# Kernel tuning notes

Hardware: AMD Instinct MI355X
Metric: run time of the kernel (lower is better)

## Reference

```python
import jax, jax.numpy as jnp
import numpy as np

F_BINS, NCH, NSRC, W, H, T, B = 257, 8, 2, 5, 32, 2000, 4
PAD = (W - 1) // 2  # use_pad=True


def setup_inputs() -> dict:
    key = jax.random.key(0)
    ks = jax.random.split(key, 7)
    s = 0.05
    return {
        "x": jax.random.normal(ks[0], (B, 2 * F_BINS, NCH, T), dtype=jnp.float32),
        # per-frequency depthwise complex conv weights: (F, Cout, Cin, w)
        "Wr1": jax.random.normal(ks[1], (F_BINS, H, NCH, W), dtype=jnp.float32) * s,
        "Wi1": jax.random.normal(ks[2], (F_BINS, H, NCH, W), dtype=jnp.float32) * s,
        "Wr2": jax.random.normal(ks[3], (F_BINS, H, H, W), dtype=jnp.float32) * s,
        "Wi2": jax.random.normal(ks[4], (F_BINS, H, H, W), dtype=jnp.float32) * s,
        "Wr3": jax.random.normal(ks[5], (F_BINS, NCH * NSRC, H, W), dtype=jnp.float32) * s,
        "Wi3": jax.random.normal(ks[6], (F_BINS, NCH * NSRC, H, W), dtype=jnp.float32) * s,
    }


def _dwconv(z, Wt):
    # z: (B, F, Cin, T) treated as NCHW with C=F, H=Cin, W=T
    # Wt: (F, Cout, Cin, w) -> grouped conv with groups=F, kernel spans full Cin
    f, cout, cin, w = Wt.shape
    k = Wt.reshape(f * cout, 1, cin, w)
    y = jax.lax.conv_general_dilated(
        z, k, window_strides=(1, 1), padding=[(0, 0), (PAD, PAD)],
        feature_group_count=f, dimension_numbers=("NCHW", "OIHW", "NCHW"))
    b = z.shape[0]
    return y.reshape(b, f, cout, -1)  # (B, F, Cout, T)


def _cconv(zr, zi, Wr, Wi):
    # complex conv: (Wr + i Wi) * (zr + i zi)
    hr = _dwconv(zr, Wr) - _dwconv(zi, Wi)
    hi = _dwconv(zr, Wi) + _dwconv(zi, Wr)
    return hr, hi


def reference(x, Wr1, Wi1, Wr2, Wi2, Wr3, Wi3):
    xr, xi = jnp.split(x, 2, axis=1)  # each (B, F, nCH, T)
    h1r, h1i = _cconv(xr, xi, Wr1, Wi1)
    h1r, h1i = jax.nn.relu(h1r), jax.nn.relu(h1i)
    h2r, h2i = _cconv(h1r, h1i, Wr2, Wi2)
    h2r, h2i = jax.nn.relu(h2r), jax.nn.relu(h2i)
    h3r, h3i = _cconv(h2r, h2i, Wr3, Wi3)  # (B, F, nCH*nSource, T)
    b, f, _, t = xr.shape
    hr = h3r.reshape(b, f, NCH, NSRC, t)
    hi = h3i.reshape(b, f, NCH, NSRC, t)
    # broadcast-multiply and reduce over channels (nCH)
    yrr = jnp.einsum("bfct,bfcst->bfst", xr, hr)
    yri = jnp.einsum("bfct,bfcst->bfst", xr, hi)
    yir = jnp.einsum("bfct,bfcst->bfst", xi, hr)
    yii = jnp.einsum("bfct,bfcst->bfst", xi, hi)
    Yr = yrr - yii
    Yi = yri + yir
    out = jnp.concatenate((Yr, Yi), axis=1)  # (B, 2F, nSource, T); squeeze is a no-op for B>1
    return jnp.squeeze(out)
```

## Files before the change

### kernel.cpp

```cpp
#include <hip/hip_runtime.h>

#define F_BINS 257
#define NCH    8
#define NSRC   2
#define KW     5
#define HCH    32
#define TLEN   2000
#define BATCH  4

#define TT      128
#define NTILES  16

#define XSTRIDE 24
#define XCOLS   148
#define XOFF    0
#define XSZ     (XCOLS * XSTRIDE * 2)
#define HWIN    144
#define H1OFF   XSZ
#define HSZ     (HWIN * 64 * 2)
#define H2OFF   (H1OFF + HSZ)
#define SMEM_BYTES (H2OFF + HSZ)
#define H3OFF   H1OFF
#define H3STRIDE 40

#define NFRAG   36
#define PW_HALF8_PER_F (NFRAG * 2 * 64)
#define PW_BYTES ((size_t)F_BINS * PW_HALF8_PER_F * 16)

typedef _Float16 half8  __attribute__((ext_vector_type(8)));
typedef __fp16   pk16x2 __attribute__((ext_vector_type(2)));
typedef float    f32x4  __attribute__((ext_vector_type(4)));

#define MFMA16(a, b, c) __builtin_amdgcn_mfma_f32_16x16x32_f16(a, b, c, 0, 0, 0)

__device__ __forceinline__ half8 gather_frag(
    int f, int frag, int mw, int lane,
    const float* __restrict__ Wr1, const float* __restrict__ Wi1,
    const float* __restrict__ Wr2, const float* __restrict__ Wi2,
    const float* __restrict__ Wr3, const float* __restrict__ Wi3)
{
    const int g = lane >> 4, r16 = lane & 15;
    half8 v;
    if (frag < 6) {
        int hr = frag / 3, p = frag % 3;
        int tap = 2 * p + (g >> 1);
        #pragma unroll
        for (int j = 0; j < 8; ++j) {
            float val = 0.f;
            if (tap < KW) {
                long idx = (((long)f * HCH + hr * 16 + r16) * NCH + j) * KW + tap;
                if (mw == 0) val = (g & 1) ? -Wi1[idx] : Wr1[idx];
                else         val = (g & 1) ?  Wr1[idx] : Wi1[idx];
            }
            v[j] = (_Float16)val;
        }
    } else if (frag < 26) {
        int u = frag - 6;
        int w = u >> 2, hr = (u >> 1) & 1, kk = u & 1;
        #pragma unroll
        for (int j = 0; j < 8; ++j) {
            int c = g * 8 + j;
            long idx = (((long)f * HCH + hr * 16 + r16) * HCH + c) * KW + w;
            float val;
            if (mw == 0) val = kk ? -Wi2[idx] : Wr2[idx];
            else         val = kk ?  Wr2[idx] : Wi2[idx];
            v[j] = (_Float16)val;
        }
    } else {
        int u = frag - 26;
        int w = u >> 1, kk = u & 1;
        #pragma unroll
        for (int j = 0; j < 8; ++j) {
            int c = g * 8 + j;
            long idx = (((long)f * (NCH * NSRC) + r16) * HCH + c) * KW + w;
            float val;
            if (mw == 0) val = kk ? -Wi3[idx] : Wr3[idx];
            else         val = kk ?  Wr3[idx] : Wi3[idx];
            v[j] = (_Float16)val;
        }
    }
    return v;
}

__global__ __launch_bounds__(256) void repack_kernel(
    const float* __restrict__ Wr1, const float* __restrict__ Wi1,
    const float* __restrict__ Wr2, const float* __restrict__ Wi2,
    const float* __restrict__ Wr3, const float* __restrict__ Wi3,
    _Float16* __restrict__ pw)
{
    const int bid  = blockIdx.x;
    const int f    = bid >> 2;
    const int part = bid & 3;
    const int lane = threadIdx.x & 63;
    const int q    = threadIdx.x >> 6;
    half8* pwv = (half8*)pw;
    for (int u = part * 18 + q; u < part * 18 + 18; u += 4) {
        int frag = u >> 1, mw = u & 1;
        half8 v = gather_frag(f, frag, mw, lane, Wr1, Wi1, Wr2, Wi2, Wr3, Wi3);
        pwv[((size_t)f * (NFRAG * 2) + u) * 64 + lane] = v;
    }
}

template<bool PACKED>
__global__ __launch_bounds__(256, 3) void cddcnn_mfma_kernel(
    const float* __restrict__ x,
    const float* __restrict__ Wr1, const float* __restrict__ Wi1,
    const float* __restrict__ Wr2, const float* __restrict__ Wi2,
    const float* __restrict__ Wr3, const float* __restrict__ Wi3,
    float* __restrict__ out, const _Float16* __restrict__ pw)
{
    __shared__ __align__(16) char sm[SMEM_BYTES];

    const int tid  = threadIdx.x;
    const int lane = tid & 63;
    const int wv   = tid >> 6;
    const int mw   = wv >> 1;
    const int nw   = wv & 1;
    const int g    = lane >> 4;
    const int r16  = lane & 15;

    const int bid = blockIdx.x;
    const int tl  = bid % NTILES;
    const int f   = (bid / NTILES) % F_BINS;
    const int b   = bid / (NTILES * F_BINS);
    const int t0  = tl * TT;

    const int nb0 = nw ? 5 : 0;
    const int nbn = nw ? 4 : 5;

    const half8* pwf = PACKED ? ((const half8*)pw) + (size_t)f * PW_HALF8_PER_F + mw * 64 + lane
                              : nullptr;
    #define LOADFRAG(fr) (PACKED ? pwf[(fr) * 128] \
                                 : gather_frag(f, (fr), mw, lane, Wr1, Wi1, Wr2, Wi2, Wr3, Wi3))

    const long xr_base = ((long)(b * 2 * F_BINS + f) * NCH) * TLEN;
    const long xi_base = ((long)(b * 2 * F_BINS + F_BINS + f) * NCH) * TLEN;

    half8 a1[2][3];
    #pragma unroll
    for (int hr = 0; hr < 2; ++hr)
    #pragma unroll
    for (int p = 0; p < 3; ++p)
        a1[hr][p] = LOADFRAG(hr * 3 + p);

    for (int u = tid; u < 16 * 37; u += 256) {
        int pc  = u / 37;
        int q   = u - pc * 37;
        int idx = q * 4;
        int tt  = t0 - 10 + idx;
        long base = (pc < 8) ? (xr_base + (long)pc * TLEN)
                             : (xi_base + (long)(pc - 8) * TLEN);
        char* wp = sm + XOFF + (idx * XSTRIDE + pc) * 2;
        #pragma unroll
        for (int h = 0; h < 2; ++h) {
            int t2 = tt + 2 * h;
            float v0 = 0.f, v1 = 0.f;
            if (t2 >= 0 && t2 + 1 < TLEN) {
                float2 xx = *(const float2*)(x + base + t2);
                v0 = xx.x; v1 = xx.y;
            } else {
                if (t2 >= 0 && t2 < TLEN)         v0 = x[base + t2];
                if (t2 + 1 >= 0 && t2 + 1 < TLEN) v1 = x[base + t2 + 1];
            }
            pk16x2 hv = __builtin_amdgcn_cvt_pkrtz(v0, v1);
            *(__fp16*)(wp + (2 * h)     * (XSTRIDE * 2)) = hv[0];
            *(__fp16*)(wp + (2 * h + 1) * (XSTRIDE * 2)) = hv[1];
        }
    }
    __syncthreads();

    const int Xc = (r16 & 7) << 4;
    int woff[2][2];
    #pragma unroll
    for (int hr = 0; hr < 2; ++hr)
    #pragma unroll
    for (int q = 0; q < 2; ++q)
        woff[hr][q] = ((mw * 64 + hr * 32 + g * 8 + q * 4) ^ Xc);

    half8 a2[5][2][2];

    {
        f32x4 acc[2][5] = {};

        #pragma unroll
        for (int w = 0; w < 2; ++w)
        #pragma unroll
        for (int hr = 0; hr < 2; ++hr)
        #pragma unroll
        for (int kk = 0; kk < 2; ++kk)
            a2[w][hr][kk] = LOADFRAG(6 + w * 4 + hr * 2 + kk);

        const char* xb = sm + XOFF + ((nb0 * 16 + r16) * XSTRIDE + (g & 1) * 8) * 2;
        #pragma unroll
        for (int p = 0; p < 3; ++p) {
            int tap = 2 * p + (g >> 1);
            if (tap > 4) tap = 4;
            const char* xbp = xb + tap * (XSTRIDE * 2);
            #pragma unroll
            for (int nbi = 0; nbi < 5; ++nbi) {
                if (nbi < nbn) {
                    const half8 bf = *(const half8*)(xbp + nbi * (16 * XSTRIDE * 2));
                    acc[0][nbi] = MFMA16(a1[0][p], bf, acc[0][nbi]);
                    acc[1][nbi] = MFMA16(a1[1][p], bf, acc[1][nbi]);
                }
            }
        }

        #pragma unroll
        for (int w = 2; w < 5; ++w)
        #pragma unroll
        for (int hr = 0; hr < 2; ++hr)
        #pragma unroll
        for (int kk = 0; kk < 2; ++kk)
            a2[w][hr][kk] = LOADFRAG(6 + w * 4 + hr * 2 + kk);

        char* wb = sm + H1OFF + (nb0 * 16 + r16) * 128;
        #pragma unroll
        for (int nbi = 0; nbi < 5; ++nbi) {
            if (nbi < nbn) {
                int t = t0 - 8 + nb0 * 16 + r16 + nbi * 16;
                bool ok = (t >= 0) && (t < TLEN);
                #pragma unroll
                for (int hr = 0; hr < 2; ++hr)
                #pragma unroll
                for (int q = 0; q < 2; ++q) {
                    float v0 = ok ? fmaxf(acc[hr][nbi][2 * q],     0.f) : 0.f;
                    float v1 = ok ? fmaxf(acc[hr][nbi][2 * q + 1], 0.f) : 0.f;
                    pk16x2 hv = __builtin_amdgcn_cvt_pkrtz(v0, v1);
                    *(pk16x2*)(wb + nbi * 2048 + woff[hr][q]) = hv;
                }
            }
        }
    }
    __syncthreads();

    half8 a3[5][2];

    {
        f32x4 acc[2][5] = {};
        #pragma unroll
        for (int w = 0; w < KW; ++w) {
            const int sc0 = nb0 * 16 + r16 + w - 2;
            const int vb  = sc0 * 128 + ((g * 16) ^ ((sc0 & 7) << 4));
            #pragma unroll
            for (int kk = 0; kk < 2; ++kk) {
                const char* rb = sm + H1OFF + (kk ? (vb ^ 64) : vb);
                #pragma unroll
                for (int nbi = 0; nbi < 5; ++nbi) {
                    if (nbi < nbn) {
                        const half8 bf = *(const half8*)(rb + nbi * 2048);
                        acc[0][nbi] = MFMA16(a2[w][0][kk], bf, acc[0][nbi]);
                        acc[1][nbi] = MFMA16(a2[w][1][kk], bf, acc[1][nbi]);
                    }
                }
            }
        }

        #pragma unroll
        for (int w = 0; w < KW; ++w)
        #pragma unroll
        for (int kk = 0; kk < 2; ++kk)
            a3[w][kk] = LOADFRAG(26 + w * 2 + kk);

        char* wb = sm + H2OFF + (nb0 * 16 + r16) * 128;
        #pragma unroll
        for (int nbi = 0; nbi < 5; ++nbi) {
            if (nbi < nbn) {
                int t = t0 - 8 + nb0 * 16 + r16 + nbi * 16;
                bool ok = (t >= 0) && (t < TLEN);
                #pragma unroll
                for (int hr = 0; hr < 2; ++hr)
                #pragma unroll
                for (int q = 0; q < 2; ++q) {
                    float v0 = ok ? fmaxf(acc[hr][nbi][2 * q],     0.f) : 0.f;
                    float v1 = ok ? fmaxf(acc[hr][nbi][2 * q + 1], 0.f) : 0.f;
                    pk16x2 hv = __builtin_amdgcn_cvt_pkrtz(v0, v1);
                    *(pk16x2*)(wb + nbi * 2048 + woff[hr][q]) = hv;
                }
            }
        }
    }
    __syncthreads();

    {
        f32x4 acc3[4] = {};
        #pragma unroll
        for (int w = 0; w < KW; ++w) {
            const int sc0 = nw * 64 + r16 + 6 + w;
            const int vb  = sc0 * 128 + ((g * 16) ^ ((sc0 & 7) << 4));
            #pragma unroll
            for (int kk = 0; kk < 2; ++kk) {
                const char* rb = sm + H2OFF + (kk ? (vb ^ 64) : vb);
                #pragma unroll
                for (int nbi = 0; nbi < 4; ++nbi) {
                    const half8 bf = *(const half8*)(rb + nbi * 2048);
                    acc3[nbi] = MFMA16(a3[w][kk], bf, acc3[nbi]);
                }
            }
        }
        char* wb3 = sm + H3OFF + (nw * 64 + r16) * (H3STRIDE * 2) + mw * 32 + g * 8;
        #pragma unroll
        for (int nbi = 0; nbi < 4; ++nbi)
        #pragma unroll
        for (int q = 0; q < 2; ++q) {
            pk16x2 hv = __builtin_amdgcn_cvt_pkrtz(acc3[nbi][2 * q], acc3[nbi][2 * q + 1]);
            *(pk16x2*)(wb3 + nbi * (16 * H3STRIDE * 2) + q * 4) = hv;
        }
    }
    __syncthreads();

    {
        int s   = tid >> 7;
        int col = tid & 127;
        int t = t0 + col;
        if (t < TLEN) {
            const half8 xrv = *(const half8*)(sm + XOFF + ((col + 10) * XSTRIDE + 0) * 2);
            const half8 xiv = *(const half8*)(sm + XOFF + ((col + 10) * XSTRIDE + 8) * 2);
            half8 h3q[4];
            #pragma unroll
            for (int q = 0; q < 4; ++q)
                h3q[q] = *(const half8*)(sm + H3OFF + col * (H3STRIDE * 2) + q * 16);
            float Yr = 0.f, Yi = 0.f;
            #pragma unroll
            for (int c = 0; c < NCH; ++c) {
                float vr = (float)xrv[c];
                float vi = (float)xiv[c];
                int o = 2 * c + s;
                float hr = (c < 4) ? (float)h3q[0][o] : (float)h3q[1][o - 8];
                float hi = (c < 4) ? (float)h3q[2][o] : (float)h3q[3][o - 8];
                Yr += vr * hr - vi * hi;
                Yi += vr * hi + vi * hr;
            }
            out[((long)(b * 2 * F_BINS + f) * NSRC + s) * TLEN + t]          = Yr;
            out[((long)(b * 2 * F_BINS + F_BINS + f) * NSRC + s) * TLEN + t] = Yi;
        }
    }
}

extern "C" void kernel_launch(void* const* d_in, const int* in_sizes, int n_in,
                              void* d_out, int out_size, void* d_ws, size_t ws_size,
                              hipStream_t stream) {
    const float* x   = (const float*)d_in[0];
    const float* Wr1 = (const float*)d_in[1];
    const float* Wi1 = (const float*)d_in[2];
    const float* Wr2 = (const float*)d_in[3];
    const float* Wi2 = (const float*)d_in[4];
    const float* Wr3 = (const float*)d_in[5];
    const float* Wi3 = (const float*)d_in[6];
    float* out = (float*)d_out;

    dim3 block(256);
    dim3 grid(BATCH * F_BINS * NTILES);
    if (ws_size >= PW_BYTES) {
        _Float16* pw = (_Float16*)d_ws;
        repack_kernel<<<F_BINS * 4, block, 0, stream>>>(Wr1, Wi1, Wr2, Wi2, Wr3, Wi3, pw);
        cddcnn_mfma_kernel<true><<<grid, block, 0, stream>>>(
            x, Wr1, Wi1, Wr2, Wi2, Wr3, Wi3, out, pw);
    } else {
        cddcnn_mfma_kernel<false><<<grid, block, 0, stream>>>(
            x, Wr1, Wi1, Wr2, Wi2, Wr3, Wi3, out, nullptr);
    }
}
```

Baseline: 256.4 us.

## Alias X staging with H2 buffer and raise occupancy to four blocks per CU

Shrinks the shared-memory footprint by letting the fp16 X tile share space with the layer-2 buffer. The final mixing stage no longer reads X from LDS; it reloads x from global memory in fp32, issuing the loads before the layer-3 MFMA loop to hide their latency. Launch bounds rise to allow four blocks per CU. The X staging loop is also rewritten so each thread packs one time column across channels. The trade-off is extra global traffic for the reload, higher register pressure from holding 16 floats per thread, and less-coalesced strided per-thread loads during staging.

```diff
diff --git a/kernel.cpp b/kernel.cpp
--- a/kernel.cpp
+++ b/kernel.cpp
@@ -13,14 +13,13 @@
 
 #define XSTRIDE 24
 #define XCOLS   148
-#define XOFF    0
-#define XSZ     (XCOLS * XSTRIDE * 2)
 #define HWIN    144
-#define H1OFF   XSZ
 #define HSZ     (HWIN * 64 * 2)
-#define H2OFF   (H1OFF + HSZ)
-#define SMEM_BYTES (H2OFF + HSZ)
-#define H3OFF   H1OFF
+#define H1OFF   0
+#define XOFF    HSZ
+#define H2OFF   HSZ
+#define H3OFF   0
+#define SMEM_BYTES (HSZ + HSZ)
 #define H3STRIDE 40
 
 #define NFRAG   36
@@ -102,7 +101,7 @@
 }
 
 template<bool PACKED>
-__global__ __launch_bounds__(256, 3) void cddcnn_mfma_kernel(
+__global__ __launch_bounds__(256, 4) void cddcnn_mfma_kernel(
     const float* __restrict__ x,
     const float* __restrict__ Wr1, const float* __restrict__ Wi1,
     const float* __restrict__ Wr2, const float* __restrict__ Wi2,
@@ -143,29 +142,19 @@
     for (int p = 0; p < 3; ++p)
         a1[hr][p] = LOADFRAG(hr * 3 + p);
 
-    for (int u = tid; u < 16 * 37; u += 256) {
-        int pc  = u / 37;
-        int q   = u - pc * 37;
-        int idx = q * 4;
-        int tt  = t0 - 10 + idx;
-        long base = (pc < 8) ? (xr_base + (long)pc * TLEN)
-                             : (xi_base + (long)(pc - 8) * TLEN);
-        char* wp = sm + XOFF + (idx * XSTRIDE + pc) * 2;
-        #pragma unroll
-        for (int h = 0; h < 2; ++h) {
-            int t2 = tt + 2 * h;
-            float v0 = 0.f, v1 = 0.f;
-            if (t2 >= 0 && t2 + 1 < TLEN) {
-                float2 xx = *(const float2*)(x + base + t2);
-                v0 = xx.x; v1 = xx.y;
-            } else {
-                if (t2 >= 0 && t2 < TLEN)         v0 = x[base + t2];
-                if (t2 + 1 >= 0 && t2 + 1 < TLEN) v1 = x[base + t2 + 1];
-            }
-            pk16x2 hv = __builtin_amdgcn_cvt_pkrtz(v0, v1);
-            *(__fp16*)(wp + (2 * h)     * (XSTRIDE * 2)) = hv[0];
-            *(__fp16*)(wp + (2 * h + 1) * (XSTRIDE * 2)) = hv[1];
-        }
+    if (tid < XCOLS) {
+        int t = t0 - 10 + tid;
+        bool ok = (t >= 0) && (t < TLEN);
+        half8 pkr, pki;
+        #pragma unroll
+        for (int c = 0; c < 8; ++c) {
+            float vr = ok ? x[xr_base + (long)c * TLEN + t] : 0.f;
+            float vi = ok ? x[xi_base + (long)c * TLEN + t] : 0.f;
+            pkr[c] = (_Float16)vr;
+            pki[c] = (_Float16)vi;
+        }
+        *(half8*)(sm + XOFF + tid * (XSTRIDE * 2))      = pkr;
+        *(half8*)(sm + XOFF + tid * (XSTRIDE * 2) + 16) = pki;
     }
     __syncthreads();
 
@@ -282,6 +271,18 @@
     }
     __syncthreads();
 
+    float mvr[8], mvi[8];
+    {
+        int colm = tid & 127;
+        int t = t0 + colm;
+        bool okm = t < TLEN;
+        #pragma unroll
+        for (int c = 0; c < 8; ++c) {
+            mvr[c] = okm ? x[xr_base + (long)c * TLEN + t] : 0.f;
+            mvi[c] = okm ? x[xi_base + (long)c * TLEN + t] : 0.f;
+        }
+    }
+
     {
         f32x4 acc3[4] = {};
         #pragma unroll
@@ -314,8 +315,6 @@
         int col = tid & 127;
         int t = t0 + col;
         if (t < TLEN) {
-            const half8 xrv = *(const half8*)(sm + XOFF + ((col + 10) * XSTRIDE + 0) * 2);
-            const half8 xiv = *(const half8*)(sm + XOFF + ((col + 10) * XSTRIDE + 8) * 2);
             half8 h3q[4];
             #pragma unroll
             for (int q = 0; q < 4; ++q)
@@ -323,13 +322,11 @@
             float Yr = 0.f, Yi = 0.f;
             #pragma unroll
             for (int c = 0; c < NCH; ++c) {
-                float vr = (float)xrv[c];
-                float vi = (float)xiv[c];
                 int o = 2 * c + s;
                 float hr = (c < 4) ? (float)h3q[0][o] : (float)h3q[1][o - 8];
                 float hi = (c < 4) ? (float)h3q[2][o] : (float)h3q[3][o - 8];
-                Yr += vr * hr - vi * hi;
-                Yi += vr * hi + vi * hr;
+                Yr += mvr[c] * hr - mvi[c] * hi;
+                Yi += mvr[c] * hi + mvi[c] * hr;
             }
             out[((long)(b * 2 * F_BINS + f) * NSRC + s) * TLEN + t]          = Yr;
             out[((long)(b * 2 * F_BINS + F_BINS + f) * NSRC + s) * TLEN + t] = Yi;
```

Measured after the change: 354.5 us. 1.38x slower.
